# Kernel optimization log

Measured on AMD Instinct MI355X. Metric: run time of the kernel, lower is better.

The kernel has to match this reference:

```python
import jax, jax.numpy as jnp
import numpy as np

N_NODES = 100000
IN_FEATS = 512
H_FEATS = 128
N_HOPS = 3
N_NIE = N_HOPS + 1  # 4 per-hop branches
N_EDGES = 1600000


def _layernorm(z, g, b, eps=1e-5):
    mu = jnp.mean(z, axis=-1, keepdims=True)
    var = jnp.var(z, axis=-1, keepdims=True)
    return (z - mu) * jax.lax.rsqrt(var + eps) * g + b


def _mlp(z, W, b, g, be):
    # Dropout(p=0) -> Linear -> LayerNorm -> ReLU (eval mode)
    return jax.nn.relu(_layernorm(z @ W + b, g, be))


def setup_inputs() -> dict:
    key = jax.random.key(0)
    ks = jax.random.split(key, 16)
    ei = jax.random.randint(ks[0], (2, N_EDGES), 0, N_NODES, dtype=jnp.int64)
    feats = jax.random.normal(ks[1], (N_NODES, IN_FEATS), dtype=jnp.float32)
    s_in = 1.0 / np.sqrt(IN_FEATS)
    s_h = 1.0 / np.sqrt(H_FEATS)
    s_c = 1.0 / np.sqrt(N_NIE * H_FEATS)
    return {
        "edge_index": ei,
        "features": feats,
        # unified input transform (transform_first=True): in_feats -> h_feats
        "W_uni": jax.random.normal(ks[2], (IN_FEATS, H_FEATS), jnp.float32) * s_in,
        "b_uni": jnp.zeros((H_FEATS,), jnp.float32),
        "g_uni": jnp.ones((H_FEATS,), jnp.float32),
        "be_uni": jnp.zeros((H_FEATS,), jnp.float32),
        # per-hop independent embeddings: h_feats -> h_feats, one per hop (stacked)
        "W_ind": jax.random.normal(ks[3], (N_NIE, H_FEATS, H_FEATS), jnp.float32) * s_h,
        "b_ind": jnp.zeros((N_NIE, H_FEATS), jnp.float32),
        "g_ind": jnp.ones((N_NIE, H_FEATS), jnp.float32),
        "be_ind": jnp.zeros((N_NIE, H_FEATS), jnp.float32),
        # relation network (RN='concat'): ndim_fc -> h_feats
        "W_rel": jax.random.normal(ks[4], (N_NIE * H_FEATS, H_FEATS), jnp.float32) * s_c,
        "b_rel": jnp.zeros((H_FEATS,), jnp.float32),
        "g_rel": jnp.ones((H_FEATS,), jnp.float32),
        "be_rel": jnp.zeros((H_FEATS,), jnp.float32),
    }


def reference(edge_index, features, W_uni, b_uni, g_uni, be_uni,
              W_ind, b_ind, g_ind, be_ind, W_rel, b_rel, g_rel, be_rel):
    N = features.shape[0]
    # F.normalize(features, dim=1)  (row_normalized=True)
    x = features / jnp.maximum(
        jnp.linalg.norm(features, axis=1, keepdims=True), 1e-12)

    # preprocess_adj: add self loops, then symmetric normalization D^-1/2 A D^-1/2
    loops = jnp.arange(N, dtype=edge_index.dtype)
    row = jnp.concatenate([edge_index[0], loops])
    col = jnp.concatenate([edge_index[1], loops])
    deg = jax.ops.segment_sum(jnp.ones_like(row, dtype=x.dtype), row,
                              num_segments=N)
    dinv = jnp.where(deg > 0, deg ** -0.5, 0.0)
    w = dinv[row] * dinv[col]  # [E+N] edge weights

    def spmm(z):
        # out[row] += w * z[col]   (gather + scatter-add, memory-bound)
        return jax.ops.segment_sum(w[:, None] * z[col], row, num_segments=N)

    # transform_first: unified embedding before multi-hop aggregation
    h = _mlp(x, W_uni, b_uni, g_uni, be_uni)  # [N, H]

    # inceptive aggregation: hop-0 is h itself, hop-i = A^i h; per-hop MLPs
    z = h
    ns = [_mlp(z, W_ind[0], b_ind[0], g_ind[0], be_ind[0])]
    for i in range(1, N_NIE):
        z = spmm(z)
        ns.append(_mlp(z, W_ind[i], b_ind[i], g_ind[i], be_ind[i]))

    cat = jnp.concatenate(ns, axis=1)  # [N, 4*H]
    out = _mlp(cat, W_rel, b_rel, g_rel, be_rel)  # [N, H]
    return out
```

## Files before the change

### kernel.cpp

```cpp
#include <hip/hip_runtime.h>
#include <hip/hip_bf16.h>

#define NN 100000
#define FE 512
#define HF 128
#define NE 1600000
#define NNIE 4

typedef __attribute__((ext_vector_type(8))) __bf16 bf16x8;
typedef __attribute__((ext_vector_type(4))) float f32x4;
typedef __attribute__((ext_vector_type(8))) unsigned short ushort8;

__device__ __forceinline__ unsigned short f2bf(float f) {
    unsigned u = __float_as_uint(f);
    unsigned r = (u + 0x7fffu + ((u >> 16) & 1u)) >> 16;
    return (unsigned short)r;
}
__device__ __forceinline__ float b2f(unsigned short u) {
    return __uint_as_float(((unsigned)u) << 16);
}

__global__ __launch_bounds__(256) void k_zero(int* __restrict__ deg,
                                              int* __restrict__ cursor, int n) {
    int i = blockIdx.x * 256 + threadIdx.x;
    if (i < n) { deg[i] = 0; cursor[i] = 0; }
}

__global__ __launch_bounds__(256) void k_count(const int* __restrict__ row,
                                               int* __restrict__ deg, int e) {
    int i = blockIdx.x * 256 + threadIdx.x;
    if (i < e) atomicAdd(&deg[row[i]], 1);
}

__global__ __launch_bounds__(1024) void k_scan1(const int* __restrict__ cnt,
                                                int* __restrict__ off,
                                                int* __restrict__ bsum,
                                                float* __restrict__ dinv,
                                                int n) {
    __shared__ int wsum[16];
    const int tid = threadIdx.x, lane = tid & 63, wid = tid >> 6;
    const int i = blockIdx.x * 1024 + tid;
    const int v = (i < n) ? cnt[i] : 0;
    if (i < n) dinv[i] = rsqrtf((float)(v + 1));
    int x = v;
#pragma unroll
    for (int s = 1; s < 64; s <<= 1) {
        int t = __shfl_up(x, s);
        if (lane >= s) x += t;
    }
    if (lane == 63) wsum[wid] = x;
    __syncthreads();
    if (wid == 0 && lane < 16) {
        int t = wsum[lane];
#pragma unroll
        for (int s = 1; s < 16; s <<= 1) {
            int u = __shfl_up(t, s);
            if (lane >= s) t += u;
        }
        wsum[lane] = t;
    }
    __syncthreads();
    const int wexc = (wid == 0) ? 0 : wsum[wid - 1];
    if (i < n) off[i] = wexc + x - v;
    if (tid == 0) bsum[blockIdx.x] = wsum[15];
}
__global__ __launch_bounds__(1024) void k_scan2(int* __restrict__ bsum, int nb,
                                                int* __restrict__ total_out) {
    __shared__ int wsum[16];
    const int tid = threadIdx.x, lane = tid & 63, wid = tid >> 6;
    const int v = (tid < nb) ? bsum[tid] : 0;
    int x = v;
#pragma unroll
    for (int s = 1; s < 64; s <<= 1) {
        int t = __shfl_up(x, s);
        if (lane >= s) x += t;
    }
    if (lane == 63) wsum[wid] = x;
    __syncthreads();
    if (wid == 0 && lane < 16) {
        int t = wsum[lane];
#pragma unroll
        for (int s = 1; s < 16; s <<= 1) {
            int u = __shfl_up(t, s);
            if (lane >= s) t += u;
        }
        wsum[lane] = t;
    }
    __syncthreads();
    const int wexc = (wid == 0) ? 0 : wsum[wid - 1];
    if (tid < nb) bsum[tid] = wexc + x - v;
    if (tid == 0) *total_out = wsum[15];
}
__global__ __launch_bounds__(256) void k_scan3(int* __restrict__ off,
                                               const int* __restrict__ bsum,
                                               int n) {
    int i = blockIdx.x * 256 + threadIdx.x;
    if (i < n) off[i] += bsum[i >> 10];
}

__global__ __launch_bounds__(256) void k_fill(const int* __restrict__ rows,
                                              const int* __restrict__ cols,
                                              const float* __restrict__ dinv,
                                              const int* __restrict__ off,
                                              int* __restrict__ cursor,
                                              int2* __restrict__ es, int e) {
    int i = blockIdx.x * 256 + threadIdx.x;
    if (i < e) {
        int r = rows[i], c = cols[i];
        int pos = off[r] + atomicAdd(&cursor[r], 1);
        es[pos] = make_int2(c, __float_as_int(dinv[r] * dinv[c]));
    }
}

__global__ __launch_bounds__(256) void k_wt_all(
    const float* __restrict__ Wu, const float* __restrict__ Wr,
    const float* __restrict__ Wi, unsigned short* __restrict__ Tu,
    unsigned short* __restrict__ Tr, unsigned short* __restrict__ Ti) {
    int i = blockIdx.x * 256 + threadIdx.x;
    if (i < 65536) {
        int k = i >> 7, n = i & 127;
        Tu[n * 512 + k] = f2bf(Wu[i]);
    } else if (i < 131072) {
        int j = i - 65536;
        int k = j >> 7, n = j & 127;
        Tr[n * 512 + k] = f2bf(Wr[j]);
    } else if (i < 196608) {
        int j = i - 131072;
        int hh = j >> 14, r = j & 16383;
        int k = r >> 7, n = r & 127;
        Ti[hh * 16384 + n * 128 + k] = f2bf(Wi[j]);
    }
}

__global__ __launch_bounds__(256) void k_spmm(
    const unsigned short* __restrict__ z, unsigned short* __restrict__ y,
    const int* __restrict__ off, const int2* __restrict__ es,
    const float* __restrict__ dinv, int n) {
    const int node = blockIdx.x * 4 + (threadIdx.x >> 6);
    if (node >= n) return;
    const int lane = threadIdx.x & 63;
    const int g = lane >> 4;
    const int l = lane & 15;

    float acc[8];
#pragma unroll
    for (int j = 0; j < 8; j++) acc[j] = 0.0f;

    const int p0 = off[node], p1 = off[node + 1];
    int p = p0 + g;
    for (; p + 12 < p1; p += 16) {
        const int2 e0 = es[p], e1 = es[p + 4], e2 = es[p + 8], e3 = es[p + 12];
        const ushort8 t0 = *(const ushort8*)(z + (size_t)e0.x * HF + 8 * l);
        const ushort8 t1 = *(const ushort8*)(z + (size_t)e1.x * HF + 8 * l);
        const ushort8 t2 = *(const ushort8*)(z + (size_t)e2.x * HF + 8 * l);
        const ushort8 t3 = *(const ushort8*)(z + (size_t)e3.x * HF + 8 * l);
        const float w0 = __int_as_float(e0.y), w1 = __int_as_float(e1.y);
        const float w2 = __int_as_float(e2.y), w3 = __int_as_float(e3.y);
#pragma unroll
        for (int j = 0; j < 8; j++) acc[j] = fmaf(w0, b2f(t0[j]), acc[j]);
#pragma unroll
        for (int j = 0; j < 8; j++) acc[j] = fmaf(w1, b2f(t1[j]), acc[j]);
#pragma unroll
        for (int j = 0; j < 8; j++) acc[j] = fmaf(w2, b2f(t2[j]), acc[j]);
#pragma unroll
        for (int j = 0; j < 8; j++) acc[j] = fmaf(w3, b2f(t3[j]), acc[j]);
    }
    for (; p + 4 < p1; p += 8) {
        const int2 e0 = es[p], e1 = es[p + 4];
        const ushort8 t0 = *(const ushort8*)(z + (size_t)e0.x * HF + 8 * l);
        const ushort8 t1 = *(const ushort8*)(z + (size_t)e1.x * HF + 8 * l);
        const float w0 = __int_as_float(e0.y), w1 = __int_as_float(e1.y);
#pragma unroll
        for (int j = 0; j < 8; j++) acc[j] = fmaf(w0, b2f(t0[j]), acc[j]);
#pragma unroll
        for (int j = 0; j < 8; j++) acc[j] = fmaf(w1, b2f(t1[j]), acc[j]);
    }
    if (p < p1) {
        const int2 e0 = es[p];
        const ushort8 t0 = *(const ushort8*)(z + (size_t)e0.x * HF + 8 * l);
        const float w0 = __int_as_float(e0.y);
#pragma unroll
        for (int j = 0; j < 8; j++) acc[j] = fmaf(w0, b2f(t0[j]), acc[j]);
    }
    if (g == 0) {
        const float di = dinv[node];
        const ushort8 v = *(const ushort8*)(z + (size_t)node * HF + 8 * l);
        const float d2 = di * di;
#pragma unroll
        for (int j = 0; j < 8; j++) acc[j] = fmaf(d2, b2f(v[j]), acc[j]);
    }
#pragma unroll
    for (int j = 0; j < 8; j++) {
        acc[j] += __shfl_xor(acc[j], 16);
        acc[j] += __shfl_xor(acc[j], 32);
    }
    if (g == 0) {
        ushort8 o;
#pragma unroll
        for (int j = 0; j < 8; j++) o[j] = f2bf(acc[j]);
        *(ushort8*)(y + (size_t)node * HF + 8 * l) = o;
    }
}

template <int K, bool NORM, typename AT, typename OT>
__global__ __launch_bounds__(256) void gemm_mfma(
    const AT* __restrict__ A, int lda, const unsigned short* __restrict__ Wt,
    const float* __restrict__ bias, const float* __restrict__ g,
    const float* __restrict__ be, OT* __restrict__ out, int ldo, int M) {
    constexpr int LDT = 72;
    __shared__ unsigned short Ast[64][LDT];
    __shared__ unsigned short Bst[128][LDT];
    __shared__ float rn_s[64];

    const int tid = threadIdx.x;
    const int row0 = blockIdx.x * 64;
    const int w = tid >> 6;
    const int lane = tid & 63;
    const int m = lane & 15;
    const int q = lane >> 4;
    const int lrow = tid >> 2;
    const int lq = tid & 3;

    f32x4 acc[8];
#pragma unroll
    for (int t = 0; t < 8; t++) acc[t] = (f32x4){0.f, 0.f, 0.f, 0.f};

    float sumsq = 0.0f;
    const bool arow_ok = (row0 + lrow) < M;

    for (int k0 = 0; k0 < K; k0 += 64) {
        __syncthreads();
#pragma unroll
        for (int oo = 0; oo < 2; oo++) {
            const int o = lq + 4 * oo;
            ushort8 pk;
            if constexpr (sizeof(AT) == 4) {
                f32x4 a0 = (f32x4){0.f, 0.f, 0.f, 0.f}, a1 = a0;
                if (arow_ok) {
                    const float* Ap = (const float*)A +
                                      (size_t)(row0 + lrow) * lda + k0 + 8 * o;
                    a0 = *(const f32x4*)Ap;
                    a1 = *(const f32x4*)(Ap + 4);
                }
                if (NORM) {
#pragma unroll
                    for (int j = 0; j < 4; j++)
                        sumsq += a0[j] * a0[j] + a1[j] * a1[j];
                }
#pragma unroll
                for (int j = 0; j < 4; j++) {
                    pk[j] = f2bf(a0[j]);
                    pk[j + 4] = f2bf(a1[j]);
                }
            } else {
                pk = (ushort8){0, 0, 0, 0, 0, 0, 0, 0};
                if (arow_ok)
                    pk = *(const ushort8*)((const unsigned short*)A +
                                           (size_t)(row0 + lrow) * lda + k0 +
                                           8 * o);
            }
            *(ushort8*)&Ast[lrow][8 * o] = pk;
        }
        const int bn = tid >> 1;
#pragma unroll
        for (int kk = 0; kk < 4; kk++) {
            const int o = (tid & 1) + 2 * kk;
            *(ushort8*)&Bst[bn][8 * o] =
                *(const ushort8*)(Wt + (size_t)bn * K + k0 + 8 * o);
        }
        __syncthreads();
#pragma unroll
        for (int jj = 0; jj < 2; jj++) {
            bf16x8 af = *(const bf16x8*)&Ast[16 * w + m][8 * q + 32 * jj];
#pragma unroll
            for (int t = 0; t < 8; t++) {
                bf16x8 bfv = *(const bf16x8*)&Bst[16 * t + m][8 * q + 32 * jj];
                acc[t] = __builtin_amdgcn_mfma_f32_16x16x32_bf16(af, bfv,
                                                                 acc[t], 0, 0,
                                                                 0);
            }
        }
    }

    if (NORM) {
        sumsq += __shfl_xor(sumsq, 1);
        sumsq += __shfl_xor(sumsq, 2);
        if (lq == 0) rn_s[lrow] = 1.0f / fmaxf(sqrtf(sumsq), 1e-12f);
        __syncthreads();
    }

    float bb[8], gg[8], ee[8];
#pragma unroll
    for (int t = 0; t < 8; t++) {
        bb[t] = bias[16 * t + m];
        gg[t] = g[16 * t + m];
        ee[t] = be[16 * t + m];
    }
#pragma unroll
    for (int r = 0; r < 4; r++) {
        const int lrow2 = 16 * w + 4 * q + r;
        float rn = 1.0f;
        if (NORM) rn = rn_s[lrow2];
        float s1 = 0.f, s2 = 0.f;
#pragma unroll
        for (int t = 0; t < 8; t++) {
            float y = fmaf(acc[t][r], rn, bb[t]);
            s1 += y;
            s2 = fmaf(y, y, s2);
        }
#pragma unroll
        for (int mask = 1; mask <= 8; mask <<= 1) {
            s1 += __shfl_xor(s1, mask);
            s2 += __shfl_xor(s2, mask);
        }
        const float mean = s1 * (1.0f / 128.0f);
        const float var = fmaxf(s2 * (1.0f / 128.0f) - mean * mean, 0.0f);
        const float rstd = rsqrtf(var + 1e-5f);
        const int grow = row0 + lrow2;
        if (grow < M) {
#pragma unroll
            for (int t = 0; t < 8; t++) {
                float y = fmaf(acc[t][r], rn, bb[t]);
                float o = fmaxf(fmaf((y - mean) * rstd, gg[t], ee[t]), 0.0f);
                if constexpr (sizeof(OT) == 2)
                    ((unsigned short*)out)[(size_t)grow * ldo + 16 * t + m] =
                        f2bf(o);
                else
                    ((float*)out)[(size_t)grow * ldo + 16 * t + m] = o;
            }
        }
    }
}

__global__ __launch_bounds__(256) void gemm128(
    const unsigned short* __restrict__ A,
    const unsigned short* __restrict__ Wt, const float* __restrict__ bias,
    const float* __restrict__ g, const float* __restrict__ be,
    unsigned short* __restrict__ out, int ldo, int M) {
    constexpr int LDT = 136;
    __shared__ unsigned short Ast[64][LDT];
    __shared__ unsigned short Bst[128][LDT];

    const int tid = threadIdx.x;
    const int row0 = blockIdx.x * 64;
    const int w = tid >> 6;
    const int lane = tid & 63;
    const int m = lane & 15;
    const int q = lane >> 4;
    const int lrow = tid >> 2;
    const int lq = tid & 3;

    const bool arow_ok = (row0 + lrow) < M;
#pragma unroll
    for (int k = 0; k < 4; k++) {
        const int o = lq + 4 * k;
        ushort8 pk = (ushort8){0, 0, 0, 0, 0, 0, 0, 0};
        if (arow_ok)
            pk = *(const ushort8*)(A + (size_t)(row0 + lrow) * HF + 8 * o);
        *(ushort8*)&Ast[lrow][8 * o] = pk;
    }
    const int bn = tid >> 1;
#pragma unroll
    for (int k = 0; k < 8; k++) {
        const int o = (tid & 1) + 2 * k;
        *(ushort8*)&Bst[bn][8 * o] =
            *(const ushort8*)(Wt + (size_t)bn * HF + 8 * o);
    }
    __syncthreads();

    f32x4 acc[8];
#pragma unroll
    for (int t = 0; t < 8; t++) acc[t] = (f32x4){0.f, 0.f, 0.f, 0.f};
#pragma unroll
    for (int jj = 0; jj < 4; jj++) {
        bf16x8 af = *(const bf16x8*)&Ast[16 * w + m][8 * q + 32 * jj];
#pragma unroll
        for (int t = 0; t < 8; t++) {
            bf16x8 bfv = *(const bf16x8*)&Bst[16 * t + m][8 * q + 32 * jj];
            acc[t] = __builtin_amdgcn_mfma_f32_16x16x32_bf16(af, bfv, acc[t], 0,
                                                             0, 0);
        }
    }

    float bb[8], gg[8], ee[8];
#pragma unroll
    for (int t = 0; t < 8; t++) {
        bb[t] = bias[16 * t + m];
        gg[t] = g[16 * t + m];
        ee[t] = be[16 * t + m];
    }
#pragma unroll
    for (int r = 0; r < 4; r++) {
        const int lrow2 = 16 * w + 4 * q + r;
        float s1 = 0.f, s2 = 0.f;
#pragma unroll
        for (int t = 0; t < 8; t++) {
            float y = acc[t][r] + bb[t];
            s1 += y;
            s2 = fmaf(y, y, s2);
        }
#pragma unroll
        for (int mask = 1; mask <= 8; mask <<= 1) {
            s1 += __shfl_xor(s1, mask);
            s2 += __shfl_xor(s2, mask);
        }
        const float mean = s1 * (1.0f / 128.0f);
        const float var = fmaxf(s2 * (1.0f / 128.0f) - mean * mean, 0.0f);
        const float rstd = rsqrtf(var + 1e-5f);
        const int grow = row0 + lrow2;
        if (grow < M) {
#pragma unroll
            for (int t = 0; t < 8; t++) {
                float y = acc[t][r] + bb[t];
                float o = fmaxf(fmaf((y - mean) * rstd, gg[t], ee[t]), 0.0f);
                out[(size_t)grow * ldo + 16 * t + m] = f2bf(o);
            }
        }
    }
}

extern "C" void kernel_launch(void* const* d_in, const int* in_sizes, int n_in,
                              void* d_out, int out_size, void* d_ws,
                              size_t ws_size, hipStream_t stream) {
    const int* ei = (const int*)d_in[0];
    const float* feats = (const float*)d_in[1];
    const float* W_uni = (const float*)d_in[2];
    const float* b_uni = (const float*)d_in[3];
    const float* g_uni = (const float*)d_in[4];
    const float* be_uni = (const float*)d_in[5];
    const float* W_ind = (const float*)d_in[6];
    const float* b_ind = (const float*)d_in[7];
    const float* g_ind = (const float*)d_in[8];
    const float* be_ind = (const float*)d_in[9];
    const float* W_rel = (const float*)d_in[10];
    const float* b_rel = (const float*)d_in[11];
    const float* g_rel = (const float*)d_in[12];
    const float* be_rel = (const float*)d_in[13];
    float* out = (float*)d_out;

    char* p = (char*)d_ws;
    auto alloc = [&](size_t bytes) {
        void* r = (void*)p;
        p += (bytes + 255) & ~(size_t)255;
        return r;
    };
    int* deg = (int*)alloc(NN * 4);
    int* cursor = (int*)alloc(NN * 4);
    int* off = (int*)alloc((NN + 1) * 4);
    int* bsum = (int*)alloc(1024 * 4);
    int2* es = (int2*)alloc((size_t)NE * 8);
    float* dinv = (float*)alloc(NN * 4);
    unsigned short* Wt_uni = (unsigned short*)alloc(128 * FE * 2);
    unsigned short* Wt_rel = (unsigned short*)alloc(128 * (NNIE * HF) * 2);
    unsigned short* Wt_ind = (unsigned short*)alloc(NNIE * HF * HF * 2);
    unsigned short* h = (unsigned short*)alloc((size_t)NN * HF * 2);
    unsigned short* za = (unsigned short*)alloc((size_t)NN * HF * 2);
    unsigned short* zb = (unsigned short*)alloc((size_t)NN * HF * 2);
    unsigned short* cat = (unsigned short*)alloc((size_t)NN * NNIE * HF * 2);

    const int gE = (NE + 255) / 256;
    const int gN = (NN + 255) / 256;
    const int gGemm = (NN + 63) / 64;
    const int gSpmm = (NN + 3) / 4;
    const int nbScan = (NN + 1023) / 1024;
    const int* erow = ei;
    const int* ecol = ei + NE;

    k_zero<<<gN, 256, 0, stream>>>(deg, cursor, NN);
    k_count<<<gE, 256, 0, stream>>>(erow, deg, NE);
    k_scan1<<<nbScan, 1024, 0, stream>>>(deg, off, bsum, dinv, NN);
    k_scan2<<<1, 1024, 0, stream>>>(bsum, nbScan, off + NN);
    k_scan3<<<gN, 256, 0, stream>>>(off, bsum, NN);
    k_fill<<<gE, 256, 0, stream>>>(erow, ecol, dinv, off, cursor, es, NE);

    k_wt_all<<<(196608 + 255) / 256, 256, 0, stream>>>(W_uni, W_rel, W_ind,
                                                       Wt_uni, Wt_rel, Wt_ind);

    gemm_mfma<FE, true, float, unsigned short>
        <<<gGemm, 256, 0, stream>>>(feats, FE, Wt_uni, b_uni, g_uni, be_uni, h,
                                    HF, NN);
    gemm128<<<gGemm, 256, 0, stream>>>(h, Wt_ind + 0 * HF * HF, b_ind, g_ind,
                                       be_ind, cat + 0 * HF, NNIE * HF, NN);
    k_spmm<<<gSpmm, 256, 0, stream>>>(h, za, off, es, dinv, NN);
    gemm128<<<gGemm, 256, 0, stream>>>(za, Wt_ind + 1 * HF * HF, b_ind + HF,
                                       g_ind + HF, be_ind + HF, cat + 1 * HF,
                                       NNIE * HF, NN);
    k_spmm<<<gSpmm, 256, 0, stream>>>(za, zb, off, es, dinv, NN);
    gemm128<<<gGemm, 256, 0, stream>>>(zb, Wt_ind + 2 * HF * HF,
                                       b_ind + 2 * HF, g_ind + 2 * HF,
                                       be_ind + 2 * HF, cat + 2 * HF,
                                       NNIE * HF, NN);
    k_spmm<<<gSpmm, 256, 0, stream>>>(zb, za, off, es, dinv, NN);
    gemm128<<<gGemm, 256, 0, stream>>>(za, Wt_ind + 3 * HF * HF,
                                       b_ind + 3 * HF, g_ind + 3 * HF,
                                       be_ind + 3 * HF, cat + 3 * HF,
                                       NNIE * HF, NN);
    gemm_mfma<NNIE * HF, false, unsigned short, float>
        <<<gGemm, 256, 0, stream>>>(cat, NNIE * HF, Wt_rel, b_rel, g_rel,
                                    be_rel, out, HF, NN);
}
```

Baseline: 791.2 us.

## Fuse per-hop MLPs and relation MLP into one tail kernel

Replaces the four per-hop gemm128 launches and the final concat GEMM with a single k_tail kernel. For each 64-row tile it computes every hop's Linear+LayerNorm+ReLU into shared memory and immediately accumulates that slice of the relation GEMM. The intent is to avoid writing and re-reading the N×512 bf16 concat buffer and to cut launch count. In exchange the third hop output now needs its own buffer, the A operand is read directly from global memory into MFMA fragments, and there are more syncthreads and weight reloads per block.

```diff
diff --git a/kernel.cpp b/kernel.cpp
--- a/kernel.cpp
+++ b/kernel.cpp
@@ -202,11 +202,11 @@
     }
 }
 
-template <int K, bool NORM, typename AT, typename OT>
-__global__ __launch_bounds__(256) void gemm_mfma(
-    const AT* __restrict__ A, int lda, const unsigned short* __restrict__ Wt,
+__global__ __launch_bounds__(256) void gemm_uni(
+    const float* __restrict__ A, const unsigned short* __restrict__ Wt,
     const float* __restrict__ bias, const float* __restrict__ g,
-    const float* __restrict__ be, OT* __restrict__ out, int ldo, int M) {
+    const float* __restrict__ be, unsigned short* __restrict__ out, int M) {
+    constexpr int K = FE;
     constexpr int LDT = 72;
     __shared__ unsigned short Ast[64][LDT];
     __shared__ unsigned short Bst[128][LDT];
@@ -233,31 +233,20 @@
 #pragma unroll
         for (int oo = 0; oo < 2; oo++) {
             const int o = lq + 4 * oo;
+            f32x4 a0 = (f32x4){0.f, 0.f, 0.f, 0.f}, a1 = a0;
+            if (arow_ok) {
+                const float* Ap =
+                    A + (size_t)(row0 + lrow) * K + k0 + 8 * o;
+                a0 = *(const f32x4*)Ap;
+                a1 = *(const f32x4*)(Ap + 4);
+            }
+#pragma unroll
+            for (int j = 0; j < 4; j++) sumsq += a0[j] * a0[j] + a1[j] * a1[j];
             ushort8 pk;
-            if constexpr (sizeof(AT) == 4) {
-                f32x4 a0 = (f32x4){0.f, 0.f, 0.f, 0.f}, a1 = a0;
-                if (arow_ok) {
-                    const float* Ap = (const float*)A +
-                                      (size_t)(row0 + lrow) * lda + k0 + 8 * o;
-                    a0 = *(const f32x4*)Ap;
-                    a1 = *(const f32x4*)(Ap + 4);
-                }
-                if (NORM) {
-#pragma unroll
-                    for (int j = 0; j < 4; j++)
-                        sumsq += a0[j] * a0[j] + a1[j] * a1[j];
-                }
-#pragma unroll
-                for (int j = 0; j < 4; j++) {
-                    pk[j] = f2bf(a0[j]);
-                    pk[j + 4] = f2bf(a1[j]);
-                }
-            } else {
-                pk = (ushort8){0, 0, 0, 0, 0, 0, 0, 0};
-                if (arow_ok)
-                    pk = *(const ushort8*)((const unsigned short*)A +
-                                           (size_t)(row0 + lrow) * lda + k0 +
-                                           8 * o);
+#pragma unroll
+            for (int j = 0; j < 4; j++) {
+                pk[j] = f2bf(a0[j]);
+                pk[j + 4] = f2bf(a1[j]);
             }
             *(ushort8*)&Ast[lrow][8 * o] = pk;
         }
@@ -282,12 +271,10 @@
         }
     }
 
-    if (NORM) {
-        sumsq += __shfl_xor(sumsq, 1);
-        sumsq += __shfl_xor(sumsq, 2);
-        if (lq == 0) rn_s[lrow] = 1.0f / fmaxf(sqrtf(sumsq), 1e-12f);
-        __syncthreads();
-    }
+    sumsq += __shfl_xor(sumsq, 1);
+    sumsq += __shfl_xor(sumsq, 2);
+    if (lq == 0) rn_s[lrow] = 1.0f / fmaxf(sqrtf(sumsq), 1e-12f);
+    __syncthreads();
 
     float bb[8], gg[8], ee[8];
 #pragma unroll
@@ -299,8 +286,7 @@
 #pragma unroll
     for (int r = 0; r < 4; r++) {
         const int lrow2 = 16 * w + 4 * q + r;
-        float rn = 1.0f;
-        if (NORM) rn = rn_s[lrow2];
+        const float rn = rn_s[lrow2];
         float s1 = 0.f, s2 = 0.f;
 #pragma unroll
         for (int t = 0; t < 8; t++) {
@@ -322,24 +308,24 @@
             for (int t = 0; t < 8; t++) {
                 float y = fmaf(acc[t][r], rn, bb[t]);
                 float o = fmaxf(fmaf((y - mean) * rstd, gg[t], ee[t]), 0.0f);
-                if constexpr (sizeof(OT) == 2)
-                    ((unsigned short*)out)[(size_t)grow * ldo + 16 * t + m] =
-                        f2bf(o);
-                else
-                    ((float*)out)[(size_t)grow * ldo + 16 * t + m] = o;
-            }
-        }
-    }
-}
-
-__global__ __launch_bounds__(256) void gemm128(
-    const unsigned short* __restrict__ A,
-    const unsigned short* __restrict__ Wt, const float* __restrict__ bias,
-    const float* __restrict__ g, const float* __restrict__ be,
-    unsigned short* __restrict__ out, int ldo, int M) {
-    constexpr int LDT = 136;
-    __shared__ unsigned short Ast[64][LDT];
-    __shared__ unsigned short Bst[128][LDT];
+                out[(size_t)grow * HF + 16 * t + m] = f2bf(o);
+            }
+        }
+    }
+}
+
+__global__ __launch_bounds__(256) void k_tail(
+    const unsigned short* __restrict__ z0, const unsigned short* __restrict__ z1,
+    const unsigned short* __restrict__ z2, const unsigned short* __restrict__ z3,
+    const unsigned short* __restrict__ Wt_ind,
+    const float* __restrict__ b_ind, const float* __restrict__ g_ind,
+    const float* __restrict__ be_ind,
+    const unsigned short* __restrict__ Wt_rel,
+    const float* __restrict__ b_rel, const float* __restrict__ g_rel,
+    const float* __restrict__ be_rel, float* __restrict__ out, int M) {
+    constexpr int LDW = 136;
+    __shared__ unsigned short Wst[128][LDW];
+    __shared__ unsigned short nsT[64][LDW];
 
     const int tid = threadIdx.x;
     const int row0 = blockIdx.x * 64;
@@ -347,47 +333,103 @@
     const int lane = tid & 63;
     const int m = lane & 15;
     const int q = lane >> 4;
-    const int lrow = tid >> 2;
-    const int lq = tid & 3;
-
-    const bool arow_ok = (row0 + lrow) < M;
-#pragma unroll
-    for (int k = 0; k < 4; k++) {
-        const int o = lq + 4 * k;
-        ushort8 pk = (ushort8){0, 0, 0, 0, 0, 0, 0, 0};
-        if (arow_ok)
-            pk = *(const ushort8*)(A + (size_t)(row0 + lrow) * HF + 8 * o);
-        *(ushort8*)&Ast[lrow][8 * o] = pk;
-    }
     const int bn = tid >> 1;
-#pragma unroll
-    for (int k = 0; k < 8; k++) {
-        const int o = (tid & 1) + 2 * k;
-        *(ushort8*)&Bst[bn][8 * o] =
-            *(const ushort8*)(Wt + (size_t)bn * HF + 8 * o);
-    }
-    __syncthreads();
-
-    f32x4 acc[8];
-#pragma unroll
-    for (int t = 0; t < 8; t++) acc[t] = (f32x4){0.f, 0.f, 0.f, 0.f};
-#pragma unroll
-    for (int jj = 0; jj < 4; jj++) {
-        bf16x8 af = *(const bf16x8*)&Ast[16 * w + m][8 * q + 32 * jj];
+
+    const unsigned short* zs[4] = {z0, z1, z2, z3};
+
+    f32x4 acc2[8];
+#pragma unroll
+    for (int t = 0; t < 8; t++) acc2[t] = (f32x4){0.f, 0.f, 0.f, 0.f};
+
+    int arow = row0 + 16 * w + m;
+    if (arow >= M) arow = M - 1;
+
+#pragma unroll
+    for (int hop = 0; hop < NNIE; hop++) {
+        __syncthreads();
+        const unsigned short* Wi = Wt_ind + hop * HF * HF;
+#pragma unroll
+        for (int k = 0; k < 8; k++) {
+            const int o = (tid & 1) + 2 * k;
+            *(ushort8*)&Wst[bn][8 * o] =
+                *(const ushort8*)(Wi + (size_t)bn * HF + 8 * o);
+        }
+        __syncthreads();
+        f32x4 acc[8];
+#pragma unroll
+        for (int t = 0; t < 8; t++) acc[t] = (f32x4){0.f, 0.f, 0.f, 0.f};
+        const unsigned short* zp = zs[hop] + (size_t)arow * HF;
+#pragma unroll
+        for (int jj = 0; jj < 4; jj++) {
+            bf16x8 af = *(const bf16x8*)(zp + 8 * q + 32 * jj);
+#pragma unroll
+            for (int t = 0; t < 8; t++) {
+                bf16x8 bfv = *(const bf16x8*)&Wst[16 * t + m][8 * q + 32 * jj];
+                acc[t] = __builtin_amdgcn_mfma_f32_16x16x32_bf16(af, bfv,
+                                                                 acc[t], 0, 0,
+                                                                 0);
+            }
+        }
+        float bb[8], gg[8], ee[8];
 #pragma unroll
         for (int t = 0; t < 8; t++) {
-            bf16x8 bfv = *(const bf16x8*)&Bst[16 * t + m][8 * q + 32 * jj];
-            acc[t] = __builtin_amdgcn_mfma_f32_16x16x32_bf16(af, bfv, acc[t], 0,
-                                                             0, 0);
+            bb[t] = b_ind[hop * HF + 16 * t + m];
+            gg[t] = g_ind[hop * HF + 16 * t + m];
+            ee[t] = be_ind[hop * HF + 16 * t + m];
+        }
+#pragma unroll
+        for (int r = 0; r < 4; r++) {
+            const int lrow2 = 16 * w + 4 * q + r;
+            float s1 = 0.f, s2 = 0.f;
+#pragma unroll
+            for (int t = 0; t < 8; t++) {
+                float y = acc[t][r] + bb[t];
+                s1 += y;
+                s2 = fmaf(y, y, s2);
+            }
+#pragma unroll
+            for (int mask = 1; mask <= 8; mask <<= 1) {
+                s1 += __shfl_xor(s1, mask);
+                s2 += __shfl_xor(s2, mask);
+            }
+            const float mean = s1 * (1.0f / 128.0f);
+            const float var = fmaxf(s2 * (1.0f / 128.0f) - mean * mean, 0.0f);
+            const float rstd = rsqrtf(var + 1e-5f);
+#pragma unroll
+            for (int t = 0; t < 8; t++) {
+                float y = acc[t][r] + bb[t];
+                float o = fmaxf(fmaf((y - mean) * rstd, gg[t], ee[t]), 0.0f);
+                nsT[lrow2][16 * t + m] = f2bf(o);
+            }
+        }
+        __syncthreads();
+#pragma unroll
+        for (int k = 0; k < 8; k++) {
+            const int o = (tid & 1) + 2 * k;
+            *(ushort8*)&Wst[bn][8 * o] =
+                *(const ushort8*)(Wt_rel + (size_t)bn * (NNIE * HF) +
+                                  HF * hop + 8 * o);
+        }
+        __syncthreads();
+#pragma unroll
+        for (int jj = 0; jj < 4; jj++) {
+            bf16x8 af = *(const bf16x8*)&nsT[16 * w + m][8 * q + 32 * jj];
+#pragma unroll
+            for (int t = 0; t < 8; t++) {
+                bf16x8 bfv = *(const bf16x8*)&Wst[16 * t + m][8 * q + 32 * jj];
+                acc2[t] = __builtin_amdgcn_mfma_f32_16x16x32_bf16(af, bfv,
+                                                                  acc2[t], 0,
+                                                                  0, 0);
+            }
         }
     }
 
     float bb[8], gg[8], ee[8];
 #pragma unroll
     for (int t = 0; t < 8; t++) {
-        bb[t] = bias[16 * t + m];
-        gg[t] = g[16 * t + m];
-        ee[t] = be[16 * t + m];
+        bb[t] = b_rel[16 * t + m];
+        gg[t] = g_rel[16 * t + m];
+        ee[t] = be_rel[16 * t + m];
     }
 #pragma unroll
     for (int r = 0; r < 4; r++) {
@@ -395,7 +437,7 @@
         float s1 = 0.f, s2 = 0.f;
 #pragma unroll
         for (int t = 0; t < 8; t++) {
-            float y = acc[t][r] + bb[t];
+            float y = acc2[t][r] + bb[t];
             s1 += y;
             s2 = fmaf(y, y, s2);
         }
@@ -411,9 +453,9 @@
         if (grow < M) {
 #pragma unroll
             for (int t = 0; t < 8; t++) {
-                float y = acc[t][r] + bb[t];
+                float y = acc2[t][r] + bb[t];
                 float o = fmaxf(fmaf((y - mean) * rstd, gg[t], ee[t]), 0.0f);
-                out[(size_t)grow * ldo + 16 * t + m] = f2bf(o);
+                out[(size_t)grow * HF + 16 * t + m] = o;
             }
         }
     }
@@ -456,7 +498,7 @@
     unsigned short* h = (unsigned short*)alloc((size_t)NN * HF * 2);
     unsigned short* za = (unsigned short*)alloc((size_t)NN * HF * 2);
     unsigned short* zb = (unsigned short*)alloc((size_t)NN * HF * 2);
-    unsigned short* cat = (unsigned short*)alloc((size_t)NN * NNIE * HF * 2);
+    unsigned short* zc = (unsigned short*)alloc((size_t)NN * HF * 2);
 
     const int gE = (NE + 255) / 256;
     const int gN = (NN + 255) / 256;
@@ -476,26 +518,13 @@
     k_wt_all<<<(196608 + 255) / 256, 256, 0, stream>>>(W_uni, W_rel, W_ind,
                                                        Wt_uni, Wt_rel, Wt_ind);
 
-    gemm_mfma<FE, true, float, unsigned short>
-        <<<gGemm, 256, 0, stream>>>(feats, FE, Wt_uni, b_uni, g_uni, be_uni, h,
-                                    HF, NN);
-    gemm128<<<gGemm, 256, 0, stream>>>(h, Wt_ind + 0 * HF * HF, b_ind, g_ind,
-                                       be_ind, cat + 0 * HF, NNIE * HF, NN);
+    gemm_uni<<<gGemm, 256, 0, stream>>>(feats, Wt_uni, b_uni, g_uni, be_uni, h,
+                                        NN);
     k_spmm<<<gSpmm, 256, 0, stream>>>(h, za, off, es, dinv, NN);
-    gemm128<<<gGemm, 256, 0, stream>>>(za, Wt_ind + 1 * HF * HF, b_ind + HF,
-                                       g_ind + HF, be_ind + HF, cat + 1 * HF,
-                                       NNIE * HF, NN);
     k_spmm<<<gSpmm, 256, 0, stream>>>(za, zb, off, es, dinv, NN);
-    gemm128<<<gGemm, 256, 0, stream>>>(zb, Wt_ind + 2 * HF * HF,
-                                       b_ind + 2 * HF, g_ind + 2 * HF,
-                                       be_ind + 2 * HF, cat + 2 * HF,
-                                       NNIE * HF, NN);
-    k_spmm<<<gSpmm, 256, 0, stream>>>(zb, za, off, es, dinv, NN);
-    gemm128<<<gGemm, 256, 0, stream>>>(za, Wt_ind + 3 * HF * HF,
-                                       b_ind + 3 * HF, g_ind + 3 * HF,
-                                       be_ind + 3 * HF, cat + 3 * HF,
-                                       NNIE * HF, NN);
-    gemm_mfma<NNIE * HF, false, unsigned short, float>
-        <<<gGemm, 256, 0, stream>>>(cat, NNIE * HF, Wt_rel, b_rel, g_rel,
-                                    be_rel, out, HF, NN);
-}
+    k_spmm<<<gSpmm, 256, 0, stream>>>(zb, zc, off, es, dinv, NN);
+
+    k_tail<<<gGemm, 256, 0, stream>>>(h, za, zb, zc, Wt_ind, b_ind, g_ind,
+                                      be_ind, Wt_rel, b_rel, g_rel, be_rel,
+                                      out, NN);
+}
```

Result: faster. 765.4 us (-3.3%).
